# Performance work log

Measured on AMD Instinct MI355X. Metric: run time of the kernel, lower is better.

Reference implementation:

```python
import jax, jax.numpy as jnp
import numpy as np

H = 1024
NH = 16
HD = H // NH
EPS = 1e-5

def setup_inputs() -> dict:
    key = jax.random.key(0)
    ks = jax.random.split(key, 5)
    B, S = 2, 2048
    scale = 1.0 / np.sqrt(H)
    return {
        "x": jax.random.normal(ks[0], (B, S, H), dtype=jnp.float32),
        "Wq": jax.random.normal(ks[1], (H, H), dtype=jnp.float32) * scale,
        "Wk": jax.random.normal(ks[2], (H, H), dtype=jnp.float32) * scale,
        "Wv": jax.random.normal(ks[3], (H, H), dtype=jnp.float32) * scale,
        "Wo": jax.random.normal(ks[4], (H, H), dtype=jnp.float32) * scale,
        "bo": jnp.zeros((H,), dtype=jnp.float32),
        "gamma": jnp.ones((H,), dtype=jnp.float32),
        "beta": jnp.zeros((H,), dtype=jnp.float32),
    }

def reference(x, Wq, Wk, Wv, Wo, bo, gamma, beta):
    B, S, _ = x.shape
    residual = x
    # pre-LayerNorm
    mu = jnp.mean(x, axis=-1, keepdims=True)
    var = jnp.mean(jnp.square(x - mu), axis=-1, keepdims=True)
    xn = (x - mu) * jax.lax.rsqrt(var + EPS) * gamma + beta
    # QKV projections (torch Linear: y = x @ W.T), split heads -> [B, NH, S, HD]
    q = (xn @ Wq.T).reshape(B, S, NH, HD).transpose(0, 2, 1, 3)
    k = (xn @ Wk.T).reshape(B, S, NH, HD).transpose(0, 2, 1, 3)
    v = (xn @ Wv.T).reshape(B, S, NH, HD).transpose(0, 2, 1, 3)
    # naive attention: explicit [B, NH, S, S] scores
    scale = 1.0 / np.sqrt(HD)
    scores = jnp.einsum('bhqd,bhkd->bhqk', q, k) * scale
    attn = jax.nn.softmax(scores.astype(jnp.float32), axis=-1).astype(q.dtype)
    out = jnp.einsum('bhqk,bhkd->bhqd', attn, v)
    out = out.transpose(0, 2, 1, 3).reshape(B, S, H)
    out = out @ Wo.T + bo
    return out + residual
```

## Files before the change

kernel.cpp:

```cpp
#include <hip/hip_runtime.h>
#include <hip/hip_bf16.h>

#define H 1024
#define NHEAD 16
#define HDIM 64
#define SEQ 2048
#define BATCH 2
#define M_TOT (BATCH * SEQ)
#define NQKV 3072

typedef __attribute__((ext_vector_type(8))) short bf16x8;
typedef __attribute__((ext_vector_type(4))) float f32x4;

#define C2_SCALE 0.18033688f

__device__ __forceinline__ unsigned short f2bf(float f) {
  union { float f; unsigned int u; } a;
  a.f = f;
  unsigned int u = a.u;
  return (unsigned short)((u + 0x7fffu + ((u >> 16) & 1u)) >> 16);
}

__device__ __forceinline__ unsigned int pkbf(float a, float b) {
  union { __hip_bfloat162 h; unsigned int u; } cv;
  cv.h = __float22bfloat162_rn(float2{a, b});
  return cv.u;
}

__device__ __forceinline__ float fast_exp2(float x) {
#if defined(__has_builtin) && __has_builtin(__builtin_amdgcn_exp2f)
  return __builtin_amdgcn_exp2f(x);
#else
  return exp2f(x);
#endif
}

typedef const __attribute__((address_space(1))) void* gas1_t;
typedef __attribute__((address_space(3))) void* las3_t;
__device__ __forceinline__ void gload16(const void* g, void* l) {
  __builtin_amdgcn_global_load_lds((gas1_t)(unsigned long long)g,
                                   (las3_t)(unsigned int)(unsigned long long)l,
                                   16, 0, 0);
}

__global__ __launch_bounds__(256) void ln_cast_kernel(const float* __restrict__ x,
                                                      const float* __restrict__ gamma,
                                                      const float* __restrict__ beta,
                                                      unsigned short* __restrict__ xn,
                                                      const float* __restrict__ w0,
                                                      const float* __restrict__ w1,
                                                      const float* __restrict__ w2,
                                                      const float* __restrict__ w3,
                                                      unsigned short* __restrict__ wdst) {
  const int t = threadIdx.x;
  if (blockIdx.x >= M_TOT) {
    const int cb = blockIdx.x - M_TOT;
    const int y = cb >> 10;
    const float* s = (y == 0) ? w0 : (y == 1) ? w1 : (y == 2) ? w2 : w3;
    const int i = (cb & 1023) * 256 + t;
    const float4 v = ((const float4*)s)[i];
    ushort4 o;
    o.x = f2bf(v.x);
    o.y = f2bf(v.y);
    o.z = f2bf(v.z);
    o.w = f2bf(v.w);
    ((ushort4*)(wdst + (size_t)y * H * H))[i] = o;
    return;
  }
  const int row = blockIdx.x;
  const float* xr = x + (size_t)row * H;
  float4 v = ((const float4*)xr)[t];
  float s = v.x + v.y + v.z + v.w;
  float s2 = v.x * v.x + v.y * v.y + v.z * v.z + v.w * v.w;
#pragma unroll
  for (int o = 32; o; o >>= 1) {
    s += __shfl_xor(s, o, 64);
    s2 += __shfl_xor(s2, o, 64);
  }
  __shared__ float red[8];
  const int wave = t >> 6;
  if ((t & 63) == 0) {
    red[wave] = s;
    red[wave + 4] = s2;
  }
  __syncthreads();
  const float ts = red[0] + red[1] + red[2] + red[3];
  const float ts2 = red[4] + red[5] + red[6] + red[7];
  const float mu = ts * (1.0f / (float)H);
  const float var = ts2 * (1.0f / (float)H) - mu * mu;
  const float rstd = rsqrtf(var + 1e-5f);
  const float4 g = ((const float4*)gamma)[t];
  const float4 b = ((const float4*)beta)[t];
  ushort4 o;
  o.x = f2bf((v.x - mu) * rstd * g.x + b.x);
  o.y = f2bf((v.y - mu) * rstd * g.y + b.y);
  o.z = f2bf((v.z - mu) * rstd * g.z + b.z);
  o.w = f2bf((v.w - mu) * rstd * g.w + b.w);
  ((ushort4*)(xn + (size_t)row * H))[t] = o;
}

template <int EPI, int NPX>
__global__ __launch_bounds__(256, 4) void gemm128(const unsigned short* __restrict__ A,
                                                  const unsigned short* __restrict__ W,
                                                  unsigned short* __restrict__ qk,
                                                  unsigned short* __restrict__ vt,
                                                  const float* __restrict__ bo,
                                                  const float* __restrict__ x,
                                                  float* __restrict__ out) {
  const int id = blockIdx.x;
  const int xcd = id & 7;
  const int r = id >> 3;
  const int nb = xcd * NPX + (r % NPX);
  const int mb = r / NPX;
  const int m0 = mb * 128;
  const int n0 = nb * 128;
  const int tid = threadIdx.x;
  const int wave = tid >> 6;
  const int lane = tid & 63;
  const int l16 = lane & 15;
  const int quad = lane >> 4;
  const int wx = wave & 1, wy = wave >> 1;

  __shared__ __align__(16) unsigned short As[2][128 * 32];
  __shared__ __align__(16) unsigned short Bs[2][128 * 32];

  const int sub = lane >> 2;
  const int kcol = (lane & 3) * 8;
  const unsigned short* ag = A + (size_t)(m0 + wave * 32 + sub) * H + kcol;
  const unsigned short* bg = W + (size_t)(n0 + wave * 32 + sub) * H + kcol;
  const int lofs = wave * 32 * 32;

  f32x4 acc[4][4] = {};

  gload16(ag, &As[0][lofs]);
  gload16(ag + 16 * H, &As[0][lofs + 16 * 32]);
  gload16(bg, &Bs[0][lofs]);
  gload16(bg + 16 * H, &Bs[0][lofs + 16 * 32]);

  for (int it = 0; it < H / 32; it++) {
    const int bi = it & 1;
    __syncthreads();
    if (it + 1 < H / 32) {
      const int k1 = (it + 1) * 32;
      gload16(ag + k1, &As[bi ^ 1][lofs]);
      gload16(ag + k1 + 16 * H, &As[bi ^ 1][lofs + 16 * 32]);
      gload16(bg + k1, &Bs[bi ^ 1][lofs]);
      gload16(bg + k1 + 16 * H, &Bs[bi ^ 1][lofs + 16 * 32]);
    }
    bf16x8 af[4], bf[4];
#pragma unroll
    for (int t = 0; t < 4; t++) {
      af[t] = *(const bf16x8*)&As[bi][(wy * 64 + t * 16 + l16) * 32 + quad * 8];
      bf[t] = *(const bf16x8*)&Bs[bi][(wx * 64 + t * 16 + l16) * 32 + quad * 8];
    }
#pragma unroll
    for (int i = 0; i < 4; i++)
#pragma unroll
      for (int j = 0; j < 4; j++)
        acc[i][j] = __builtin_amdgcn_mfma_f32_16x16x32_bf16(af[i], bf[j], acc[i][j], 0, 0, 0);
  }

  if (EPI == 0) {
#pragma unroll
    for (int j = 0; j < 4; j++) {
      const int cb = n0 + wx * 64 + j * 16;
      if (cb < 2048) {
        const float qs = (cb < 1024) ? C2_SCALE : 1.0f;
#pragma unroll
        for (int i = 0; i < 4; i++) {
          const int row = m0 + wy * 64 + i * 16 + quad * 4;
#pragma unroll
          for (int r2 = 0; r2 < 4; r2++)
            qk[(size_t)(row + r2) * 2048 + cb + l16] = f2bf(acc[i][j][r2] * qs);
        }
      } else {
        const int n = cb + l16 - 2048;
#pragma unroll
        for (int i = 0; i < 4; i++) {
          const int row0 = m0 + wy * 64 + i * 16 + quad * 4;
          const int b = row0 >> 11;
          const int s = row0 & 2047;
          ushort4 p;
          p.x = f2bf(acc[i][j][0]);
          p.y = f2bf(acc[i][j][1]);
          p.z = f2bf(acc[i][j][2]);
          p.w = f2bf(acc[i][j][3]);
          *(ushort4*)&vt[((size_t)b * 1024 + n) * SEQ + s] = p;
        }
      }
    }
  } else {
#pragma unroll
    for (int j = 0; j < 4; j++) {
      const int col = n0 + wx * 64 + j * 16 + l16;
      const float bv = bo[col];
#pragma unroll
      for (int i = 0; i < 4; i++) {
        const int row = m0 + wy * 64 + i * 16 + quad * 4;
#pragma unroll
        for (int r2 = 0; r2 < 4; r2++) {
          const size_t idx = (size_t)(row + r2) * H + col;
          out[idx] = acc[i][j][r2] + bv + x[idx];
        }
      }
    }
  }
}

__global__ __launch_bounds__(256, 2) void attn_kernel(const unsigned short* __restrict__ qk,
                                                      const unsigned short* __restrict__ vt,
                                                      unsigned short* __restrict__ O) {
  const int id = blockIdx.x;
  const int xcd = id & 7;
  const int slot = id >> 3;
  const int qt = slot & 15;
  const int g = slot >> 4;
  const int combo = xcd * 4 + g;
  const int h = combo & 15;
  const int b = combo >> 4;
  const int tid = threadIdx.x;
  const int wave = tid >> 6;
  const int lane = tid & 63;
  const int l16 = lane & 15;
  const int quad = lane >> 4;
  const int l8 = l16 & 7;

  __shared__ __align__(16) unsigned short Kt[2][64 * 64];
  __shared__ __align__(16) unsigned short Vt[2][64 * 64];
  __shared__ __align__(16) unsigned short Pt[8][16 * 64];

  const unsigned short* Qbase = qk + (size_t)b * SEQ * 2048 + h * 64;
  const unsigned short* Kbase = qk + (size_t)b * SEQ * 2048 + 1024 + h * 64;
  const unsigned short* Vbase = vt + ((size_t)b * 1024 + h * 64) * SEQ;

  const int rIn = lane >> 3;
  const int gsw = (lane & 7) ^ rIn;
  const int ch0 = 2 * wave;

  const int qrow0 = qt * 128 + wave * 32 + l16;
  bf16x8 aq[2][2];
#pragma unroll
  for (int u = 0; u < 2; u++)
#pragma unroll
    for (int c = 0; c < 2; c++)
      aq[u][c] = *(const bf16x8*)(Qbase + (size_t)(qrow0 + u * 16) * 2048 + c * 32 + quad * 8);

  float lacc[2][2] = {};
  f32x4 o_acc[2][4] = {};

#pragma unroll
  for (int c = 0; c < 2; c++) {
    const int ch = ch0 + c;
    const int row = ch * 8 + rIn;
    gload16(Kbase + (size_t)row * 2048 + gsw * 8, &Kt[0][ch * 512]);
    gload16(Vbase + (size_t)row * SEQ + gsw * 8, &Vt[0][ch * 512]);
  }

  unsigned short* myP0 = &Pt[wave * 2 + 0][0];
  unsigned short* myP1 = &Pt[wave * 2 + 1][0];

#pragma unroll 2
  for (int it = 0; it < SEQ / 64; it++) {
    const int bi = it & 1;
    __syncthreads();
    if (it + 1 < SEQ / 64) {
#pragma unroll
      for (int c = 0; c < 2; c++) {
        const int ch = ch0 + c;
        const int row = ch * 8 + rIn;
        gload16(Kbase + (size_t)((it + 1) * 64 + row) * 2048 + gsw * 8,
                &Kt[bi ^ 1][ch * 512]);
        gload16(Vbase + (size_t)row * SEQ + (it + 1) * 64 + gsw * 8,
                &Vt[bi ^ 1][ch * 512]);
      }
    }

    f32x4 s[2][4] = {};
#pragma unroll
    for (int c = 0; c < 2; c++) {
#pragma unroll
      for (int t = 0; t < 4; t++) {
        const bf16x8 kf =
            *(const bf16x8*)&Kt[bi][(t * 16 + l16) * 64 + (((c * 4 + quad) ^ l8) * 8)];
        s[0][t] = __builtin_amdgcn_mfma_f32_16x16x32_bf16(kf, aq[0][c], s[0][t], 0, 0, 0);
        s[1][t] = __builtin_amdgcn_mfma_f32_16x16x32_bf16(kf, aq[1][c], s[1][t], 0, 0, 0);
      }
    }

    float pv[2][4][4];
#pragma unroll
    for (int u = 0; u < 2; u++)
#pragma unroll
      for (int t = 0; t < 4; t++) {
#pragma unroll
        for (int r = 0; r < 4; r++) pv[u][t][r] = fast_exp2(s[u][t][r]);
        lacc[u][t & 1] += (pv[u][t][0] + pv[u][t][1]) + (pv[u][t][2] + pv[u][t][3]);
      }

#pragma unroll
    for (int t = 0; t < 4; t++) {
      const int wofs = l16 * 64 + (((t * 2 + (quad >> 1)) ^ l8) * 8) + (quad & 1) * 4;
      uint2 d0, d1;
      d0.x = pkbf(pv[0][t][0], pv[0][t][1]);
      d0.y = pkbf(pv[0][t][2], pv[0][t][3]);
      d1.x = pkbf(pv[1][t][0], pv[1][t][1]);
      d1.y = pkbf(pv[1][t][2], pv[1][t][3]);
      *(uint2*)&myP0[wofs] = d0;
      *(uint2*)&myP1[wofs] = d1;
    }

#pragma unroll
    for (int c = 0; c < 2; c++) {
      const int rofs = l16 * 64 + (((c * 4 + quad) ^ l8) * 8);
      const bf16x8 pb0 = *(const bf16x8*)&myP0[rofs];
      const bf16x8 pb1 = *(const bf16x8*)&myP1[rofs];
#pragma unroll
      for (int dt = 0; dt < 4; dt++) {
        const bf16x8 vf =
            *(const bf16x8*)&Vt[bi][(dt * 16 + l16) * 64 + (((c * 4 + quad) ^ l8) * 8)];
        o_acc[0][dt] = __builtin_amdgcn_mfma_f32_16x16x32_bf16(vf, pb0, o_acc[0][dt], 0, 0, 0);
        o_acc[1][dt] = __builtin_amdgcn_mfma_f32_16x16x32_bf16(vf, pb1, o_acc[1][dt], 0, 0, 0);
      }
    }
  }

#pragma unroll
  for (int u = 0; u < 2; u++) {
    float l_i = lacc[u][0] + lacc[u][1];
    l_i += __shfl_xor(l_i, 16, 64);
    l_i += __shfl_xor(l_i, 32, 64);
    const float inv = 1.0f / l_i;
    unsigned short* orow = O + ((size_t)(b * SEQ + qrow0 + u * 16)) * H + h * 64;
#pragma unroll
    for (int dt = 0; dt < 4; dt++) {
      uint2 d;
      d.x = pkbf(o_acc[u][dt][0] * inv, o_acc[u][dt][1] * inv);
      d.y = pkbf(o_acc[u][dt][2] * inv, o_acc[u][dt][3] * inv);
      *(uint2*)&orow[dt * 16 + quad * 4] = d;
    }
  }
}

extern "C" void kernel_launch(void* const* d_in, const int* in_sizes, int n_in,
                              void* d_out, int out_size, void* d_ws, size_t ws_size,
                              hipStream_t stream) {
  const float* x = (const float*)d_in[0];
  const float* Wq = (const float*)d_in[1];
  const float* Wk = (const float*)d_in[2];
  const float* Wv = (const float*)d_in[3];
  const float* Wo = (const float*)d_in[4];
  const float* bo = (const float*)d_in[5];
  const float* gamma = (const float*)d_in[6];
  const float* beta = (const float*)d_in[7];
  float* out = (float*)d_out;

  unsigned short* ws = (unsigned short*)d_ws;
  unsigned short* xn = ws;
  unsigned short* wcat = xn + (size_t)M_TOT * H;
  unsigned short* wob = wcat + (size_t)3 * H * H;
  unsigned short* qkb = wcat + (size_t)4 * H * H;
  unsigned short* vtb = qkb + (size_t)M_TOT * 2048;
  unsigned short* atb = vtb + (size_t)BATCH * H * SEQ;

  ln_cast_kernel<<<M_TOT + 4096, 256, 0, stream>>>(x, gamma, beta, xn, Wq, Wk, Wv, Wo,
                                                   wcat);
  gemm128<0, 3><<<(M_TOT / 128) * (NQKV / 128), 256, 0, stream>>>(
      xn, wcat, qkb, vtb, nullptr, nullptr, nullptr);
  attn_kernel<<<(SEQ / 128) * NHEAD * BATCH, 256, 0, stream>>>(qkb, vtb, atb);
  gemm128<1, 1><<<(M_TOT / 128) * (H / 128), 256, 0, stream>>>(
      atb, wob, nullptr, nullptr, bo, x, out);
}
```

Measured before the change: 195.7 us.

## Use 32x32x16 MFMA in attention and pass P through lane shuffles instead of LDS

```diff
diff --git a/kernel.cpp b/kernel.cpp
--- a/kernel.cpp
+++ b/kernel.cpp
@@ -11,6 +11,7 @@
 
 typedef __attribute__((ext_vector_type(8))) short bf16x8;
 typedef __attribute__((ext_vector_type(4))) float f32x4;
+typedef __attribute__((ext_vector_type(16))) float f32x16;
 
 #define C2_SCALE 0.18033688f
 
@@ -221,13 +222,12 @@
   const int tid = threadIdx.x;
   const int wave = tid >> 6;
   const int lane = tid & 63;
-  const int l16 = lane & 15;
-  const int quad = lane >> 4;
-  const int l8 = l16 & 7;
+  const int l32 = lane & 31;
+  const int hh = lane >> 5;
+  const int l8 = l32 & 7;
 
   __shared__ __align__(16) unsigned short Kt[2][64 * 64];
   __shared__ __align__(16) unsigned short Vt[2][64 * 64];
-  __shared__ __align__(16) unsigned short Pt[8][16 * 64];
 
   const unsigned short* Qbase = qk + (size_t)b * SEQ * 2048 + h * 64;
   const unsigned short* Kbase = qk + (size_t)b * SEQ * 2048 + 1024 + h * 64;
@@ -237,16 +237,14 @@
   const int gsw = (lane & 7) ^ rIn;
   const int ch0 = 2 * wave;
 
-  const int qrow0 = qt * 128 + wave * 32 + l16;
-  bf16x8 aq[2][2];
-#pragma unroll
-  for (int u = 0; u < 2; u++)
-#pragma unroll
-    for (int c = 0; c < 2; c++)
-      aq[u][c] = *(const bf16x8*)(Qbase + (size_t)(qrow0 + u * 16) * 2048 + c * 32 + quad * 8);
-
-  float lacc[2][2] = {};
-  f32x4 o_acc[2][4] = {};
+  const int qrow = qt * 128 + wave * 32 + l32;
+  bf16x8 bq[4];
+#pragma unroll
+  for (int ks = 0; ks < 4; ks++)
+    bq[ks] = *(const bf16x8*)(Qbase + (size_t)qrow * 2048 + ks * 16 + hh * 8);
+
+  float lacc[2] = {0.0f, 0.0f};
+  f32x16 o_acc[2] = {};
 
 #pragma unroll
   for (int c = 0; c < 2; c++) {
@@ -255,9 +253,6 @@
     gload16(Kbase + (size_t)row * 2048 + gsw * 8, &Kt[0][ch * 512]);
     gload16(Vbase + (size_t)row * SEQ + gsw * 8, &Vt[0][ch * 512]);
   }
-
-  unsigned short* myP0 = &Pt[wave * 2 + 0][0];
-  unsigned short* myP1 = &Pt[wave * 2 + 1][0];
 
 #pragma unroll 2
   for (int it = 0; it < SEQ / 64; it++) {
@@ -275,68 +270,77 @@
       }
     }
 
-    f32x4 s[2][4] = {};
-#pragma unroll
-    for (int c = 0; c < 2; c++) {
-#pragma unroll
-      for (int t = 0; t < 4; t++) {
-        const bf16x8 kf =
-            *(const bf16x8*)&Kt[bi][(t * 16 + l16) * 64 + (((c * 4 + quad) ^ l8) * 8)];
-        s[0][t] = __builtin_amdgcn_mfma_f32_16x16x32_bf16(kf, aq[0][c], s[0][t], 0, 0, 0);
-        s[1][t] = __builtin_amdgcn_mfma_f32_16x16x32_bf16(kf, aq[1][c], s[1][t], 0, 0, 0);
-      }
-    }
-
-    float pv[2][4][4];
-#pragma unroll
-    for (int u = 0; u < 2; u++)
-#pragma unroll
-      for (int t = 0; t < 4; t++) {
-#pragma unroll
-        for (int r = 0; r < 4; r++) pv[u][t][r] = fast_exp2(s[u][t][r]);
-        lacc[u][t & 1] += (pv[u][t][0] + pv[u][t][1]) + (pv[u][t][2] + pv[u][t][3]);
-      }
-
-#pragma unroll
-    for (int t = 0; t < 4; t++) {
-      const int wofs = l16 * 64 + (((t * 2 + (quad >> 1)) ^ l8) * 8) + (quad & 1) * 4;
-      uint2 d0, d1;
-      d0.x = pkbf(pv[0][t][0], pv[0][t][1]);
-      d0.y = pkbf(pv[0][t][2], pv[0][t][3]);
-      d1.x = pkbf(pv[1][t][0], pv[1][t][1]);
-      d1.y = pkbf(pv[1][t][2], pv[1][t][3]);
-      *(uint2*)&myP0[wofs] = d0;
-      *(uint2*)&myP1[wofs] = d1;
-    }
-
-#pragma unroll
-    for (int c = 0; c < 2; c++) {
-      const int rofs = l16 * 64 + (((c * 4 + quad) ^ l8) * 8);
-      const bf16x8 pb0 = *(const bf16x8*)&myP0[rofs];
-      const bf16x8 pb1 = *(const bf16x8*)&myP1[rofs];
-#pragma unroll
-      for (int dt = 0; dt < 4; dt++) {
-        const bf16x8 vf =
-            *(const bf16x8*)&Vt[bi][(dt * 16 + l16) * 64 + (((c * 4 + quad) ^ l8) * 8)];
-        o_acc[0][dt] = __builtin_amdgcn_mfma_f32_16x16x32_bf16(vf, pb0, o_acc[0][dt], 0, 0, 0);
-        o_acc[1][dt] = __builtin_amdgcn_mfma_f32_16x16x32_bf16(vf, pb1, o_acc[1][dt], 0, 0, 0);
-      }
-    }
-  }
-
-#pragma unroll
-  for (int u = 0; u < 2; u++) {
-    float l_i = lacc[u][0] + lacc[u][1];
-    l_i += __shfl_xor(l_i, 16, 64);
-    l_i += __shfl_xor(l_i, 32, 64);
-    const float inv = 1.0f / l_i;
-    unsigned short* orow = O + ((size_t)(b * SEQ + qrow0 + u * 16)) * H + h * 64;
-#pragma unroll
-    for (int dt = 0; dt < 4; dt++) {
+    f32x16 sa[2] = {};
+#pragma unroll
+    for (int ks = 0; ks < 4; ks++) {
+#pragma unroll
+      for (int mt = 0; mt < 2; mt++) {
+        const bf16x8 kf = *(const bf16x8*)&Kt[bi][(mt * 32 + l32) * 64 +
+                                                  (((ks * 2 + hh) ^ l8) * 8)];
+        sa[mt] = __builtin_amdgcn_mfma_f32_32x32x16_bf16(kf, bq[ks], sa[mt], 0, 0, 0);
+      }
+    }
+
+    unsigned int pk[2][8];
+#pragma unroll
+    for (int mt = 0; mt < 2; mt++) {
+      float p[16];
+#pragma unroll
+      for (int r2 = 0; r2 < 16; r2++) p[r2] = fast_exp2(sa[mt][r2]);
+      float ls = 0.0f;
+#pragma unroll
+      for (int r2 = 0; r2 < 16; r2++) ls += p[r2];
+      lacc[mt] += ls;
+#pragma unroll
+      for (int q = 0; q < 8; q++) pk[mt][q] = pkbf(p[2 * q], p[2 * q + 1]);
+    }
+
+    unsigned int rcv[2][2][2];
+#pragma unroll
+    for (int mt = 0; mt < 2; mt++)
+#pragma unroll
+      for (int half = 0; half < 2; half++)
+#pragma unroll
+        for (int c = 0; c < 2; c++) {
+          const unsigned int snd =
+              hh ? pk[mt][4 * half + c] : pk[mt][4 * half + 2 + c];
+          rcv[mt][half][c] = (unsigned int)__shfl_xor((int)snd, 32, 64);
+        }
+
+#pragma unroll
+    for (int ks = 0; ks < 4; ks++) {
+      const int mt = ks >> 1;
+      const int half = ks & 1;
+      const unsigned int o0 = pk[mt][4 * half + 2 * hh + 0];
+      const unsigned int o1 = pk[mt][4 * half + 2 * hh + 1];
+      const unsigned int r0 = rcv[mt][half][0];
+      const unsigned int r1 = rcv[mt][half][1];
+      union { unsigned int w[4]; bf16x8 v; } pb;
+      pb.w[0] = hh ? r0 : o0;
+      pb.w[1] = hh ? r1 : o1;
+      pb.w[2] = hh ? o0 : r0;
+      pb.w[3] = hh ? o1 : r1;
+#pragma unroll
+      for (int dt = 0; dt < 2; dt++) {
+        const bf16x8 vf = *(const bf16x8*)&Vt[bi][(dt * 32 + l32) * 64 +
+                                                  (((ks * 2 + hh) ^ l8) * 8)];
+        o_acc[dt] = __builtin_amdgcn_mfma_f32_32x32x16_bf16(vf, pb.v, o_acc[dt], 0, 0, 0);
+      }
+    }
+  }
+
+  float l_i = lacc[0] + lacc[1];
+  l_i += __shfl_xor(l_i, 32, 64);
+  const float inv = 1.0f / l_i;
+  unsigned short* orow = O + ((size_t)(b * SEQ + qrow)) * H + h * 64;
+#pragma unroll
+  for (int dt = 0; dt < 2; dt++) {
+#pragma unroll
+    for (int s2 = 0; s2 < 4; s2++) {
       uint2 d;
-      d.x = pkbf(o_acc[u][dt][0] * inv, o_acc[u][dt][1] * inv);
-      d.y = pkbf(o_acc[u][dt][2] * inv, o_acc[u][dt][3] * inv);
-      *(uint2*)&orow[dt * 16 + quad * 4] = d;
+      d.x = pkbf(o_acc[dt][4 * s2 + 0] * inv, o_acc[dt][4 * s2 + 1] * inv);
+      d.y = pkbf(o_acc[dt][4 * s2 + 2] * inv, o_acc[dt][4 * s2 + 3] * inv);
+      *(uint2*)&orow[dt * 32 + 4 * hh + 8 * s2] = d;
     }
   }
 }
```

Result: slower. 225.5 us (+15.2%).

## Fuse all four stages into one persistent cooperative kernel with grid syncs

Applied to the files above, without the earlier changes.

```diff
diff --git a/kernel.cpp b/kernel.cpp
--- a/kernel.cpp
+++ b/kernel.cpp
@@ -1,5 +1,8 @@
 #include <hip/hip_runtime.h>
 #include <hip/hip_bf16.h>
+#include <hip/hip_cooperative_groups.h>
+
+namespace cg = cooperative_groups;
 
 #define H 1024
 #define NHEAD 16
@@ -8,6 +11,7 @@
 #define BATCH 2
 #define M_TOT (BATCH * SEQ)
 #define NQKV 3072
+#define NCOOP 512
 
 typedef __attribute__((ext_vector_type(8))) short bf16x8;
 typedef __attribute__((ext_vector_type(4))) float f32x4;
@@ -43,41 +47,40 @@
                                    16, 0, 0);
 }
 
-__global__ __launch_bounds__(256) void ln_cast_kernel(const float* __restrict__ x,
-                                                      const float* __restrict__ gamma,
-                                                      const float* __restrict__ beta,
-                                                      unsigned short* __restrict__ xn,
-                                                      const float* __restrict__ w0,
-                                                      const float* __restrict__ w1,
-                                                      const float* __restrict__ w2,
-                                                      const float* __restrict__ w3,
-                                                      unsigned short* __restrict__ wdst) {
+__device__ __forceinline__ void lncast_tile(int v, float* red, const float* __restrict__ x,
+                                            const float* __restrict__ gamma,
+                                            const float* __restrict__ beta,
+                                            unsigned short* __restrict__ xn,
+                                            const float* __restrict__ w0,
+                                            const float* __restrict__ w1,
+                                            const float* __restrict__ w2,
+                                            const float* __restrict__ w3,
+                                            unsigned short* __restrict__ wdst) {
   const int t = threadIdx.x;
-  if (blockIdx.x >= M_TOT) {
-    const int cb = blockIdx.x - M_TOT;
+  if (v >= M_TOT) {
+    const int cb = v - M_TOT;
     const int y = cb >> 10;
     const float* s = (y == 0) ? w0 : (y == 1) ? w1 : (y == 2) ? w2 : w3;
     const int i = (cb & 1023) * 256 + t;
-    const float4 v = ((const float4*)s)[i];
+    const float4 vv = ((const float4*)s)[i];
     ushort4 o;
-    o.x = f2bf(v.x);
-    o.y = f2bf(v.y);
-    o.z = f2bf(v.z);
-    o.w = f2bf(v.w);
+    o.x = f2bf(vv.x);
+    o.y = f2bf(vv.y);
+    o.z = f2bf(vv.z);
+    o.w = f2bf(vv.w);
     ((ushort4*)(wdst + (size_t)y * H * H))[i] = o;
     return;
   }
-  const int row = blockIdx.x;
+  const int row = v;
   const float* xr = x + (size_t)row * H;
-  float4 v = ((const float4*)xr)[t];
-  float s = v.x + v.y + v.z + v.w;
-  float s2 = v.x * v.x + v.y * v.y + v.z * v.z + v.w * v.w;
+  float4 vv = ((const float4*)xr)[t];
+  float s = vv.x + vv.y + vv.z + vv.w;
+  float s2 = vv.x * vv.x + vv.y * vv.y + vv.z * vv.z + vv.w * vv.w;
 #pragma unroll
   for (int o = 32; o; o >>= 1) {
     s += __shfl_xor(s, o, 64);
     s2 += __shfl_xor(s2, o, 64);
   }
-  __shared__ float red[8];
   const int wave = t >> 6;
   if ((t & 63) == 0) {
     red[wave] = s;
@@ -89,25 +92,26 @@
   const float mu = ts * (1.0f / (float)H);
   const float var = ts2 * (1.0f / (float)H) - mu * mu;
   const float rstd = rsqrtf(var + 1e-5f);
-  const float4 g = ((const float4*)gamma)[t];
-  const float4 b = ((const float4*)beta)[t];
+  const float4 gm = ((const float4*)gamma)[t];
+  const float4 bt = ((const float4*)beta)[t];
   ushort4 o;
-  o.x = f2bf((v.x - mu) * rstd * g.x + b.x);
-  o.y = f2bf((v.y - mu) * rstd * g.y + b.y);
-  o.z = f2bf((v.z - mu) * rstd * g.z + b.z);
-  o.w = f2bf((v.w - mu) * rstd * g.w + b.w);
+  o.x = f2bf((vv.x - mu) * rstd * gm.x + bt.x);
+  o.y = f2bf((vv.y - mu) * rstd * gm.y + bt.y);
+  o.z = f2bf((vv.z - mu) * rstd * gm.z + bt.z);
+  o.w = f2bf((vv.w - mu) * rstd * gm.w + bt.w);
   ((ushort4*)(xn + (size_t)row * H))[t] = o;
+  __syncthreads();
 }
 
 template <int EPI, int NPX>
-__global__ __launch_bounds__(256, 4) void gemm128(const unsigned short* __restrict__ A,
-                                                  const unsigned short* __restrict__ W,
-                                                  unsigned short* __restrict__ qk,
-                                                  unsigned short* __restrict__ vt,
-                                                  const float* __restrict__ bo,
-                                                  const float* __restrict__ x,
-                                                  float* __restrict__ out) {
-  const int id = blockIdx.x;
+__device__ __forceinline__ void gemm_tile(int id, unsigned short* As, unsigned short* Bs,
+                                          const unsigned short* __restrict__ A,
+                                          const unsigned short* __restrict__ W,
+                                          unsigned short* __restrict__ qk,
+                                          unsigned short* __restrict__ vt,
+                                          const float* __restrict__ bo,
+                                          const float* __restrict__ x,
+                                          float* __restrict__ out) {
   const int xcd = id & 7;
   const int r = id >> 3;
   const int nb = xcd * NPX + (r % NPX);
@@ -121,9 +125,6 @@
   const int quad = lane >> 4;
   const int wx = wave & 1, wy = wave >> 1;
 
-  __shared__ __align__(16) unsigned short As[2][128 * 32];
-  __shared__ __align__(16) unsigned short Bs[2][128 * 32];
-
   const int sub = lane >> 2;
   const int kcol = (lane & 3) * 8;
   const unsigned short* ag = A + (size_t)(m0 + wave * 32 + sub) * H + kcol;
@@ -132,26 +133,26 @@
 
   f32x4 acc[4][4] = {};
 
-  gload16(ag, &As[0][lofs]);
-  gload16(ag + 16 * H, &As[0][lofs + 16 * 32]);
-  gload16(bg, &Bs[0][lofs]);
-  gload16(bg + 16 * H, &Bs[0][lofs + 16 * 32]);
+  gload16(ag, &As[lofs]);
+  gload16(ag + 16 * H, &As[lofs + 16 * 32]);
+  gload16(bg, &Bs[lofs]);
+  gload16(bg + 16 * H, &Bs[lofs + 16 * 32]);
 
   for (int it = 0; it < H / 32; it++) {
     const int bi = it & 1;
     __syncthreads();
     if (it + 1 < H / 32) {
       const int k1 = (it + 1) * 32;
-      gload16(ag + k1, &As[bi ^ 1][lofs]);
-      gload16(ag + k1 + 16 * H, &As[bi ^ 1][lofs + 16 * 32]);
-      gload16(bg + k1, &Bs[bi ^ 1][lofs]);
-      gload16(bg + k1 + 16 * H, &Bs[bi ^ 1][lofs + 16 * 32]);
+      gload16(ag + k1, &As[(bi ^ 1) * 4096 + lofs]);
+      gload16(ag + k1 + 16 * H, &As[(bi ^ 1) * 4096 + lofs + 16 * 32]);
+      gload16(bg + k1, &Bs[(bi ^ 1) * 4096 + lofs]);
+      gload16(bg + k1 + 16 * H, &Bs[(bi ^ 1) * 4096 + lofs + 16 * 32]);
     }
     bf16x8 af[4], bf[4];
 #pragma unroll
     for (int t = 0; t < 4; t++) {
-      af[t] = *(const bf16x8*)&As[bi][(wy * 64 + t * 16 + l16) * 32 + quad * 8];
-      bf[t] = *(const bf16x8*)&Bs[bi][(wx * 64 + t * 16 + l16) * 32 + quad * 8];
+      af[t] = *(const bf16x8*)&As[bi * 4096 + (wy * 64 + t * 16 + l16) * 32 + quad * 8];
+      bf[t] = *(const bf16x8*)&Bs[bi * 4096 + (wx * 64 + t * 16 + l16) * 32 + quad * 8];
     }
 #pragma unroll
     for (int i = 0; i < 4; i++)
@@ -159,6 +160,7 @@
       for (int j = 0; j < 4; j++)
         acc[i][j] = __builtin_amdgcn_mfma_f32_16x16x32_bf16(af[i], bf[j], acc[i][j], 0, 0, 0);
   }
+  __syncthreads();
 
   if (EPI == 0) {
 #pragma unroll
@@ -207,10 +209,11 @@
   }
 }
 
-__global__ __launch_bounds__(256, 2) void attn_kernel(const unsigned short* __restrict__ qk,
-                                                      const unsigned short* __restrict__ vt,
-                                                      unsigned short* __restrict__ O) {
-  const int id = blockIdx.x;
+__device__ __forceinline__ void attn_tile(int id, unsigned short* Kt, unsigned short* Vt,
+                                          unsigned short* Pt,
+                                          const unsigned short* __restrict__ qk,
+                                          const unsigned short* __restrict__ vt,
+                                          unsigned short* __restrict__ O) {
   const int xcd = id & 7;
   const int slot = id >> 3;
   const int qt = slot & 15;
@@ -225,10 +228,6 @@
   const int quad = lane >> 4;
   const int l8 = l16 & 7;
 
-  __shared__ __align__(16) unsigned short Kt[2][64 * 64];
-  __shared__ __align__(16) unsigned short Vt[2][64 * 64];
-  __shared__ __align__(16) unsigned short Pt[8][16 * 64];
-
   const unsigned short* Qbase = qk + (size_t)b * SEQ * 2048 + h * 64;
   const unsigned short* Kbase = qk + (size_t)b * SEQ * 2048 + 1024 + h * 64;
   const unsigned short* Vbase = vt + ((size_t)b * 1024 + h * 64) * SEQ;
@@ -252,12 +251,12 @@
   for (int c = 0; c < 2; c++) {
     const int ch = ch0 + c;
     const int row = ch * 8 + rIn;
-    gload16(Kbase + (size_t)row * 2048 + gsw * 8, &Kt[0][ch * 512]);
-    gload16(Vbase + (size_t)row * SEQ + gsw * 8, &Vt[0][ch * 512]);
-  }
-
-  unsigned short* myP0 = &Pt[wave * 2 + 0][0];
-  unsigned short* myP1 = &Pt[wave * 2 + 1][0];
+    gload16(Kbase + (size_t)row * 2048 + gsw * 8, &Kt[ch * 512]);
+    gload16(Vbase + (size_t)row * SEQ + gsw * 8, &Vt[ch * 512]);
+  }
+
+  unsigned short* myP0 = &Pt[(wave * 2 + 0) * 1024];
+  unsigned short* myP1 = &Pt[(wave * 2 + 1) * 1024];
 
 #pragma unroll 2
   for (int it = 0; it < SEQ / 64; it++) {
@@ -269,9 +268,9 @@
         const int ch = ch0 + c;
         const int row = ch * 8 + rIn;
         gload16(Kbase + (size_t)((it + 1) * 64 + row) * 2048 + gsw * 8,
-                &Kt[bi ^ 1][ch * 512]);
+                &Kt[(bi ^ 1) * 4096 + ch * 512]);
         gload16(Vbase + (size_t)row * SEQ + (it + 1) * 64 + gsw * 8,
-                &Vt[bi ^ 1][ch * 512]);
+                &Vt[(bi ^ 1) * 4096 + ch * 512]);
       }
     }
 
@@ -280,8 +279,8 @@
     for (int c = 0; c < 2; c++) {
 #pragma unroll
       for (int t = 0; t < 4; t++) {
-        const bf16x8 kf =
-            *(const bf16x8*)&Kt[bi][(t * 16 + l16) * 64 + (((c * 4 + quad) ^ l8) * 8)];
+        const bf16x8 kf = *(const bf16x8*)&Kt[bi * 4096 + (t * 16 + l16) * 64 +
+                                              (((c * 4 + quad) ^ l8) * 8)];
         s[0][t] = __builtin_amdgcn_mfma_f32_16x16x32_bf16(kf, aq[0][c], s[0][t], 0, 0, 0);
         s[1][t] = __builtin_amdgcn_mfma_f32_16x16x32_bf16(kf, aq[1][c], s[1][t], 0, 0, 0);
       }
@@ -316,13 +315,14 @@
       const bf16x8 pb1 = *(const bf16x8*)&myP1[rofs];
 #pragma unroll
       for (int dt = 0; dt < 4; dt++) {
-        const bf16x8 vf =
-            *(const bf16x8*)&Vt[bi][(dt * 16 + l16) * 64 + (((c * 4 + quad) ^ l8) * 8)];
+        const bf16x8 vf = *(const bf16x8*)&Vt[bi * 4096 + (dt * 16 + l16) * 64 +
+                                              (((c * 4 + quad) ^ l8) * 8)];
         o_acc[0][dt] = __builtin_amdgcn_mfma_f32_16x16x32_bf16(vf, pb0, o_acc[0][dt], 0, 0, 0);
         o_acc[1][dt] = __builtin_amdgcn_mfma_f32_16x16x32_bf16(vf, pb1, o_acc[1][dt], 0, 0, 0);
       }
     }
   }
+  __syncthreads();
 
 #pragma unroll
   for (int u = 0; u < 2; u++) {
@@ -339,6 +339,71 @@
       *(uint2*)&orow[dt * 16 + quad * 4] = d;
     }
   }
+}
+
+__global__ __launch_bounds__(256, 2) void mega_kernel(
+    const float* __restrict__ x, const float* __restrict__ Wq,
+    const float* __restrict__ Wk, const float* __restrict__ Wv,
+    const float* __restrict__ Wo, const float* __restrict__ bo,
+    const float* __restrict__ gamma, const float* __restrict__ beta,
+    unsigned short* __restrict__ xn, unsigned short* __restrict__ wcat,
+    unsigned short* __restrict__ qkb, unsigned short* __restrict__ vtb,
+    unsigned short* __restrict__ atb, float* __restrict__ out) {
+  __shared__ __align__(16) unsigned short smem[24576];
+  __shared__ float red[8];
+  cg::grid_group grid = cg::this_grid();
+  const int bid = blockIdx.x;
+
+  for (int v = bid; v < M_TOT + 4096; v += NCOOP)
+    lncast_tile(v, red, x, gamma, beta, xn, Wq, Wk, Wv, Wo, wcat);
+  grid.sync();
+
+  for (int tile = bid; tile < 768; tile += NCOOP)
+    gemm_tile<0, 3>(tile, smem, smem + 8192, xn, wcat, qkb, vtb, nullptr, nullptr,
+                    nullptr);
+  grid.sync();
+
+  attn_tile(bid, smem, smem + 8192, smem + 16384, qkb, vtb, atb);
+  grid.sync();
+
+  if (bid < 256)
+    gemm_tile<1, 1>(bid, smem, smem + 8192, atb, wcat + (size_t)3 * H * H, nullptr,
+                    nullptr, bo, x, out);
+}
+
+__global__ __launch_bounds__(256) void ln_cast_kernel(const float* __restrict__ x,
+                                                      const float* __restrict__ gamma,
+                                                      const float* __restrict__ beta,
+                                                      unsigned short* __restrict__ xn,
+                                                      const float* __restrict__ w0,
+                                                      const float* __restrict__ w1,
+                                                      const float* __restrict__ w2,
+                                                      const float* __restrict__ w3,
+                                                      unsigned short* __restrict__ wdst) {
+  __shared__ float red[8];
+  lncast_tile(blockIdx.x, red, x, gamma, beta, xn, w0, w1, w2, w3, wdst);
+}
+
+template <int EPI, int NPX>
+__global__ __launch_bounds__(256, 4) void gemm128(const unsigned short* __restrict__ A,
+                                                  const unsigned short* __restrict__ W,
+                                                  unsigned short* __restrict__ qk,
+                                                  unsigned short* __restrict__ vt,
+                                                  const float* __restrict__ bo,
+                                                  const float* __restrict__ x,
+                                                  float* __restrict__ out) {
+  __shared__ __align__(16) unsigned short As[2 * 4096];
+  __shared__ __align__(16) unsigned short Bs[2 * 4096];
+  gemm_tile<EPI, NPX>(blockIdx.x, As, Bs, A, W, qk, vt, bo, x, out);
+}
+
+__global__ __launch_bounds__(256, 2) void attn_kernel(const unsigned short* __restrict__ qk,
+                                                      const unsigned short* __restrict__ vt,
+                                                      unsigned short* __restrict__ O) {
+  __shared__ __align__(16) unsigned short Kt[2 * 4096];
+  __shared__ __align__(16) unsigned short Vt[2 * 4096];
+  __shared__ __align__(16) unsigned short Pt[8192];
+  attn_tile(blockIdx.x, Kt, Vt, Pt, qk, vt, O);
 }
 
 extern "C" void kernel_launch(void* const* d_in, const int* in_sizes, int n_in,
@@ -348,25 +413,33 @@
   const float* Wq = (const float*)d_in[1];
   const float* Wk = (const float*)d_in[2];
   const float* Wv = (const float*)d_in[3];
+  const float* Wv_ = Wv;
   const float* Wo = (const float*)d_in[4];
   const float* bo = (const float*)d_in[5];
   const float* gamma = (const float*)d_in[6];
   const float* beta = (const float*)d_in[7];
   float* out = (float*)d_out;
+  (void)Wv_;
 
   unsigned short* ws = (unsigned short*)d_ws;
   unsigned short* xn = ws;
   unsigned short* wcat = xn + (size_t)M_TOT * H;
-  unsigned short* wob = wcat + (size_t)3 * H * H;
   unsigned short* qkb = wcat + (size_t)4 * H * H;
   unsigned short* vtb = qkb + (size_t)M_TOT * 2048;
   unsigned short* atb = vtb + (size_t)BATCH * H * SEQ;
 
-  ln_cast_kernel<<<M_TOT + 4096, 256, 0, stream>>>(x, gamma, beta, xn, Wq, Wk, Wv, Wo,
-                                                   wcat);
-  gemm128<0, 3><<<(M_TOT / 128) * (NQKV / 128), 256, 0, stream>>>(
-      xn, wcat, qkb, vtb, nullptr, nullptr, nullptr);
-  attn_kernel<<<(SEQ / 128) * NHEAD * BATCH, 256, 0, stream>>>(qkb, vtb, atb);
-  gemm128<1, 1><<<(M_TOT / 128) * (H / 128), 256, 0, stream>>>(
-      atb, wob, nullptr, nullptr, bo, x, out);
-}
+  void* args[] = {&x, &Wq, &Wk, &Wv, &Wo, &bo, &gamma, &beta,
+                  &xn, &wcat, &qkb, &vtb, &atb, &out};
+  hipError_t e = hipLaunchCooperativeKernel((const void*)mega_kernel, dim3(NCOOP),
+                                            dim3(256), args, 0, stream);
+  if (e != hipSuccess) {
+    (void)hipGetLastError();
+    ln_cast_kernel<<<M_TOT + 4096, 256, 0, stream>>>(x, gamma, beta, xn, Wq, Wk, Wv, Wo,
+                                                     wcat);
+    gemm128<0, 3><<<(M_TOT / 128) * (NQKV / 128), 256, 0, stream>>>(
+        xn, wcat, qkb, vtb, nullptr, nullptr, nullptr);
+    attn_kernel<<<(SEQ / 128) * NHEAD * BATCH, 256, 0, stream>>>(qkb, vtb, atb);
+    gemm128<1, 1><<<(M_TOT / 128) * (H / 128), 256, 0, stream>>>(
+        atb, wcat + (size_t)3 * H * H, nullptr, nullptr, bo, x, out);
+  }
+}
```

Measured after the change: 410.6 us. 110% more time.
